# Kernel optimization log

Measured on AMD Instinct MI355X. Metric: run time of the kernel, lower is better.

## Reference

```python
import jax, jax.numpy as jnp
import numpy as np
import math

T, B, I, N, O = 512, 256, 128, 1024, 10
H_STEP = 0.1
ALPHA = 1.0
OMEGA = 1.0
GAMMA = 0.1
OMEGA_FACTOR = OMEGA * OMEGA
GAMMA_FACTOR = 2.0 * GAMMA
GAIN_REC = 1.0 / math.sqrt(N)


def setup_inputs() -> dict:
    key = jax.random.key(0)
    ks = jax.random.split(key, 7)
    # torch.nn.Linear default init: U(-1/sqrt(fan_in), 1/sqrt(fan_in))
    def lin(kw, kb, fan_out, fan_in):
        bound = 1.0 / math.sqrt(fan_in)
        w = jax.random.uniform(kw, (fan_out, fan_in), minval=-bound, maxval=bound, dtype=jnp.float32)
        b = jax.random.uniform(kb, (fan_out,), minval=-bound, maxval=bound, dtype=jnp.float32)
        return w, b
    i2h_w, i2h_b = lin(ks[0], ks[1], N, I)
    h2h_w, h2h_b = lin(ks[2], ks[3], N, N)
    h2o_w, h2o_b = lin(ks[4], ks[5], O, N)
    batch = jax.random.normal(ks[6], (T, B, I), dtype=jnp.float32)
    return {
        "batch": batch,
        "i2h_w": i2h_w, "i2h_b": i2h_b,
        "h2h_w": h2h_w, "h2h_b": h2h_b,
        "h2o_w": h2o_w, "h2o_b": h2o_b,
    }


def reference(batch, i2h_w, i2h_b, h2h_w, h2h_b, h2o_w, h2o_b):
    # Precompute input projection for all timesteps: [T, B, N]
    inp_proj = jnp.einsum('tbi,ni->tbn', batch, i2h_w) + i2h_b

    def step(carry, u_t):
        x_t, y_t = carry  # each [B, N]
        rec = GAIN_REC * (y_t @ h2h_w.T + h2h_b)  # gain scales full h2h(y) incl. bias
        y_t = y_t + H_STEP * (ALPHA * jnp.tanh(u_t + rec)
                              - OMEGA_FACTOR * x_t - GAMMA_FACTOR * y_t)
        x_t = x_t + H_STEP * y_t
        return (x_t, y_t), None

    x0 = jnp.zeros((batch.shape[1], h2h_w.shape[0]), dtype=batch.dtype)
    y0 = jnp.zeros_like(x0)
    (x_T, _), _ = jax.lax.scan(step, (x0, y0), inp_proj)
    output = x_T @ h2o_w.T + h2o_b  # [B, O]
    return output
```

## Files before the change

kernel.cpp:

```cpp
#include <hip/hip_runtime.h>

#define T_STEPS 512
#define BATCH_N 256
#define IDIM    128
#define NDIM    1024
#define ODIM    10

#define AGRP 16
#define BSLC 16
#define BB   16
#define NS   64
#define THREADS 256
#define GAIN 0.03125f

#define BATCH_BYTES (33554432ull)
#define YBUF_OFF    (33554432ull)
#define YBUF_HALF   (524288ull)
#define SEQ_OFF     (YBUF_OFF + 2*YBUF_HALF)
#define SEQ_BYTES   (4096ull)
#define XT_OFF      (SEQ_OFF + SEQ_BYTES)
#define XT_BYTES    (1048576ull)
#define WS_NEED     (XT_OFF + XT_BYTES)

typedef short    s16x8 __attribute__((ext_vector_type(8)));
typedef float    f32x4 __attribute__((ext_vector_type(4)));
typedef unsigned u32x4 __attribute__((ext_vector_type(4)));

__device__ __forceinline__ unsigned short f2bf(float f) {
  unsigned u = __builtin_bit_cast(unsigned, f);
  u += 0x7fffu + ((u >> 16) & 1u);
  return (unsigned short)(u >> 16);
}

__global__ void horn_convert(const float* __restrict__ src, unsigned short* __restrict__ dst) {
  size_t gid = (size_t)blockIdx.x * 256 + threadIdx.x;
  const f32x4* s4 = reinterpret_cast<const f32x4*>(src) + gid * 2;
  f32x4 a = s4[0], b = s4[1];
  u32x4 o;
  o[0] = (unsigned)f2bf(a[0]) | ((unsigned)f2bf(a[1]) << 16);
  o[1] = (unsigned)f2bf(a[2]) | ((unsigned)f2bf(a[3]) << 16);
  o[2] = (unsigned)f2bf(b[0]) | ((unsigned)f2bf(b[1]) << 16);
  o[3] = (unsigned)f2bf(b[2]) | ((unsigned)f2bf(b[3]) << 16);
  reinterpret_cast<u32x4*>(dst)[gid] = o;
}

__launch_bounds__(THREADS, 1)
__global__ void horn_persistent(const unsigned short* __restrict__ batchbf,
                                const float* __restrict__ i2h_w,
                                const float* __restrict__ i2h_b,
                                const float* __restrict__ h2h_w,
                                const float* __restrict__ h2h_b,
                                unsigned short* ybuf,
                                unsigned int*  seq,
                                float* xT)
{
  __shared__ char smem[32768];
  const int tid  = threadIdx.x;
  const int lane = tid & 63;
  const int wv   = tid >> 6;
  const int blk  = blockIdx.x;
  const int ig   = blk & 15;
  const int jg   = blk >> 4;
  const int l15  = lane & 15;
  const int kb   = lane >> 4;
  const int jc   = jg * NS + wv * 16 + l15;

  s16x8 wfrag[32];
  #pragma unroll
  for (int kc = 0; kc < 32; ++kc) {
    const f32x4* g = reinterpret_cast<const f32x4*>(h2h_w + (size_t)jc * NDIM + kc * 32 + kb * 8);
    f32x4 a = g[0], b = g[1];
    s16x8 v;
    v[0] = (short)f2bf(a[0]*GAIN); v[1] = (short)f2bf(a[1]*GAIN);
    v[2] = (short)f2bf(a[2]*GAIN); v[3] = (short)f2bf(a[3]*GAIN);
    v[4] = (short)f2bf(b[0]*GAIN); v[5] = (short)f2bf(b[1]*GAIN);
    v[6] = (short)f2bf(b[2]*GAIN); v[7] = (short)f2bf(b[3]*GAIN);
    wfrag[kc] = v;
  }

  s16x8 i2hf[4];
  #pragma unroll
  for (int kc = 0; kc < 4; ++kc) {
    const float* g = i2h_w + (size_t)jc * IDIM + kc * 32 + kb * 8;
    s16x8 v;
    #pragma unroll
    for (int e = 0; e < 8; ++e) v[e] = (short)f2bf(g[e]);
    i2hf[kc] = v;
  }
  const float bias = i2h_b[jc] + h2h_b[jc] * GAIN;

  s16x8 bfr[4];
  {
    const unsigned short* bp = batchbf + ((size_t)ig * BB + l15) * IDIM + kb * 8;
    #pragma unroll
    for (int kc = 0; kc < 4; ++kc) bfr[kc] = *reinterpret_cast<const s16x8*>(bp + kc * 32);
  }

  float xs[4] = {0.f,0.f,0.f,0.f};
  float ys[4] = {0.f,0.f,0.f,0.f};
  unsigned int* cnt = seq + ig * 32;

  for (int t = 0; t < T_STEPS; ++t) {
    if (t > 0) {
      const unsigned target = 64u * (unsigned)t;
      while (true) {
        unsigned v = 0;
        if (lane == 0) v = atomicAdd(cnt, 0u);
        v = (unsigned)__shfl((int)v, 0, 64);
        if (v >= target) break;
        __builtin_amdgcn_s_sleep(1);
      }
    }

    const char* gy = (const char*)ybuf + (size_t)(t & 1) * YBUF_HALF + (size_t)ig * (BB * NDIM * 2);
    const u32x4* g4 = reinterpret_cast<const u32x4*>(gy) + tid;
    u32x4 v0, v1, v2, v3, v4, v5, v6, v7;
    asm volatile(
      "global_load_dwordx4 %0, %8, off sc0 sc1\n\t"
      "global_load_dwordx4 %1, %9, off sc0 sc1\n\t"
      "global_load_dwordx4 %2, %10, off sc0 sc1\n\t"
      "global_load_dwordx4 %3, %11, off sc0 sc1\n\t"
      "global_load_dwordx4 %4, %12, off sc0 sc1\n\t"
      "global_load_dwordx4 %5, %13, off sc0 sc1\n\t"
      "global_load_dwordx4 %6, %14, off sc0 sc1\n\t"
      "global_load_dwordx4 %7, %15, off sc0 sc1"
      : "=&v"(v0), "=&v"(v1), "=&v"(v2), "=&v"(v3),
        "=&v"(v4), "=&v"(v5), "=&v"(v6), "=&v"(v7)
      : "v"(g4), "v"(g4+256), "v"(g4+512), "v"(g4+768),
        "v"(g4+1024), "v"(g4+1280), "v"(g4+1536), "v"(g4+1792)
      : "memory");

    f32x4 acc = {bias, bias, bias, bias};
    #pragma unroll
    for (int kc = 0; kc < 4; ++kc)
      acc = __builtin_amdgcn_mfma_f32_16x16x32_bf16(bfr[kc], i2hf[kc], acc, 0, 0, 0);

    asm volatile("s_waitcnt vmcnt(0)" ::: "memory");
    #define STG(r, vr) { int idx = tid + (r)*256; \
      *reinterpret_cast<u32x4*>(smem + ((idx*16) ^ (((idx>>7)&7)<<4))) = vr; }
    STG(0, v0) STG(1, v1) STG(2, v2) STG(3, v3)
    STG(4, v4) STG(5, v5) STG(6, v6) STG(7, v7)
    #undef STG
    __syncthreads();

    {
      const int tn = (t + 1 < T_STEPS) ? (t + 1) : t;
      const unsigned short* bp = batchbf + ((size_t)tn * BATCH_N + ig * BB + l15) * IDIM + kb * 8;
      #pragma unroll
      for (int kc = 0; kc < 4; ++kc) bfr[kc] = *reinterpret_cast<const s16x8*>(bp + kc * 32);
    }

    {
      const char* ybase = smem + l15 * 2048;
      const int swz = (l15 & 7) << 4;
      #pragma unroll
      for (int kc = 0; kc < 32; ++kc) {
        int ko = kc * 64 + kb * 16;
        s16x8 a = *reinterpret_cast<const s16x8*>(ybase + (ko ^ swz));
        acc = __builtin_amdgcn_mfma_f32_16x16x32_bf16(a, wfrag[kc], acc, 0, 0, 0);
      }
    }

    unsigned yw0, yw1, yw2, yw3;
    {
      float z, th, yn;
      z = acc[0]; th = tanhf(z); yn = ys[0] + 0.1f*(th - xs[0] - 0.2f*ys[0]); xs[0] += 0.1f*yn; ys[0] = yn; yw0 = f2bf(yn);
      z = acc[1]; th = tanhf(z); yn = ys[1] + 0.1f*(th - xs[1] - 0.2f*ys[1]); xs[1] += 0.1f*yn; ys[1] = yn; yw1 = f2bf(yn);
      z = acc[2]; th = tanhf(z); yn = ys[2] + 0.1f*(th - xs[2] - 0.2f*ys[2]); xs[2] += 0.1f*yn; ys[2] = yn; yw2 = f2bf(yn);
      z = acc[3]; th = tanhf(z); yn = ys[3] + 0.1f*(th - xs[3] - 0.2f*ys[3]); xs[3] += 0.1f*yn; ys[3] = yn; yw3 = f2bf(yn);
    }

    {
      unsigned short* wp = ybuf + (size_t)((t + 1) & 1) * 262144 + (size_t)ig * (BB * NDIM) + jc;
      asm volatile(
        "global_store_short %4, %0, off sc0 sc1\n\t"
        "global_store_short %5, %1, off sc0 sc1\n\t"
        "global_store_short %6, %2, off sc0 sc1\n\t"
        "global_store_short %7, %3, off sc0 sc1\n\t"
        "s_waitcnt vmcnt(0)"
        :
        : "v"(yw0), "v"(yw1), "v"(yw2), "v"(yw3),
          "v"(wp + (size_t)(kb*4+0)*NDIM), "v"(wp + (size_t)(kb*4+1)*NDIM),
          "v"(wp + (size_t)(kb*4+2)*NDIM), "v"(wp + (size_t)(kb*4+3)*NDIM)
        : "memory");
    }
    if (lane == 0) atomicAdd(cnt, 1u);
  }

  #pragma unroll
  for (int q = 0; q < 4; ++q) {
    int row = ig * BB + kb * 4 + q;
    xT[(size_t)row * NDIM + jc] = xs[q];
  }
}

__global__ void horn_out(const float* __restrict__ xT, const float* __restrict__ h2o_w,
                         const float* __restrict__ h2o_b, float* __restrict__ out) {
  int b = blockIdx.x;
  int lane = threadIdx.x;
  float p[ODIM];
  #pragma unroll
  for (int o = 0; o < ODIM; ++o) p[o] = 0.f;
  for (int it = 0; it < NDIM / 64; ++it) {
    int n = it * 64 + lane;
    float xv = xT[(size_t)b * NDIM + n];
    #pragma unroll
    for (int o = 0; o < ODIM; ++o) p[o] += xv * h2o_w[o * NDIM + n];
  }
  #pragma unroll
  for (int o = 0; o < ODIM; ++o) {
    float v = p[o];
    #pragma unroll
    for (int off = 32; off >= 1; off >>= 1) v += __shfl_down(v, off, 64);
    if (lane == 0) out[b * ODIM + o] = v + h2o_b[o];
  }
}

__global__ void horn_fail(float* out) {
  int i = blockIdx.x * 256 + threadIdx.x;
  if (i < BATCH_N * ODIM) out[i] = 12345.0f;
}

extern "C" void kernel_launch(void* const* d_in, const int* in_sizes, int n_in,
                              void* d_out, int out_size, void* d_ws, size_t ws_size,
                              hipStream_t stream) {
  const float* batch = (const float*)d_in[0];
  const float* i2h_w = (const float*)d_in[1];
  const float* i2h_b = (const float*)d_in[2];
  const float* h2h_w = (const float*)d_in[3];
  const float* h2h_b = (const float*)d_in[4];
  const float* h2o_w = (const float*)d_in[5];
  const float* h2o_b = (const float*)d_in[6];
  float* out = (float*)d_out;
  char* ws = (char*)d_ws;

  if (ws_size < WS_NEED) {
    horn_fail<<<16, 256, 0, stream>>>(out);
    return;
  }

  hipMemsetAsync(ws + YBUF_OFF, 0, YBUF_HALF, stream);
  hipMemsetAsync(ws + SEQ_OFF, 0, SEQ_BYTES, stream);

  horn_convert<<<8192, 256, 0, stream>>>(batch, (unsigned short*)(ws + 0));

  horn_persistent<<<AGRP * BSLC, THREADS, 0, stream>>>(
      (const unsigned short*)(ws + 0), i2h_w, i2h_b, h2h_w, h2h_b,
      (unsigned short*)(ws + YBUF_OFF), (unsigned int*)(ws + SEQ_OFF),
      (float*)(ws + XT_OFF));

  horn_out<<<BATCH_N, 64, 0, stream>>>((const float*)(ws + XT_OFF), h2o_w, h2o_b, out);
}
```

Baseline: 1.583 ms.

## Split recurrent K across waves with LDS reduction and per-wave flag barrier

Each wave now covers a quarter of the K dimension for all 64 output columns of the block. It loads its y slice straight from global memory into MFMA operands, skipping the LDS staging copy, and partial sums are reduced through a double-buffered LDS array. The shared atomic counter barrier is replaced by per-wave flag words that all 64 lanes poll together, so the atomic read-modify-write and the sleep are gone. tanhf is replaced by an exp/rcp formulation. Together these aim to shorten each recurrent step's critical path of sync, load and compute, at the cost of an extra LDS reduction and slightly lower tanh accuracy.

Result: slower. 4.251 ms (+168.6%).

```diff
diff --git a/kernel.cpp b/kernel.cpp
--- a/kernel.cpp
+++ b/kernel.cpp
@@ -6,19 +6,16 @@
 #define NDIM    1024
 #define ODIM    10
 
-#define AGRP 16
-#define BSLC 16
 #define BB   16
 #define NS   64
 #define THREADS 256
 #define GAIN 0.03125f
 
-#define BATCH_BYTES (33554432ull)
 #define YBUF_OFF    (33554432ull)
 #define YBUF_HALF   (524288ull)
-#define SEQ_OFF     (YBUF_OFF + 2*YBUF_HALF)
-#define SEQ_BYTES   (4096ull)
-#define XT_OFF      (SEQ_OFF + SEQ_BYTES)
+#define FLG_OFF     (YBUF_OFF + 2*YBUF_HALF)
+#define FLG_BYTES   (4096ull)
+#define XT_OFF      (FLG_OFF + FLG_BYTES)
 #define XT_BYTES    (1048576ull)
 #define WS_NEED     (XT_OFF + XT_BYTES)
 
@@ -51,10 +48,10 @@
                                 const float* __restrict__ h2h_w,
                                 const float* __restrict__ h2h_b,
                                 unsigned short* ybuf,
-                                unsigned int*  seq,
+                                unsigned int*  flags,
                                 float* xT)
 {
-  __shared__ char smem[32768];
+  __shared__ f32x4 red[2][16][64];
   const int tid  = threadIdx.x;
   const int lane = tid & 63;
   const int wv   = tid >> 6;
@@ -65,17 +62,21 @@
   const int kb   = lane >> 4;
   const int jc   = jg * NS + wv * 16 + l15;
 
-  s16x8 wfrag[32];
-  #pragma unroll
-  for (int kc = 0; kc < 32; ++kc) {
-    const f32x4* g = reinterpret_cast<const f32x4*>(h2h_w + (size_t)jc * NDIM + kc * 32 + kb * 8);
-    f32x4 a = g[0], b = g[1];
-    s16x8 v;
-    v[0] = (short)f2bf(a[0]*GAIN); v[1] = (short)f2bf(a[1]*GAIN);
-    v[2] = (short)f2bf(a[2]*GAIN); v[3] = (short)f2bf(a[3]*GAIN);
-    v[4] = (short)f2bf(b[0]*GAIN); v[5] = (short)f2bf(b[1]*GAIN);
-    v[6] = (short)f2bf(b[2]*GAIN); v[7] = (short)f2bf(b[3]*GAIN);
-    wfrag[kc] = v;
+  s16x8 wfrag[4][8];
+  #pragma unroll
+  for (int ct = 0; ct < 4; ++ct) {
+    #pragma unroll
+    for (int q = 0; q < 8; ++q) {
+      const float* g = h2h_w + (size_t)(jg * NS + ct * 16 + l15) * NDIM + wv * 256 + q * 32 + kb * 8;
+      f32x4 a = *reinterpret_cast<const f32x4*>(g);
+      f32x4 b = *reinterpret_cast<const f32x4*>(g + 4);
+      s16x8 v;
+      v[0] = (short)f2bf(a[0]*GAIN); v[1] = (short)f2bf(a[1]*GAIN);
+      v[2] = (short)f2bf(a[2]*GAIN); v[3] = (short)f2bf(a[3]*GAIN);
+      v[4] = (short)f2bf(b[0]*GAIN); v[5] = (short)f2bf(b[1]*GAIN);
+      v[6] = (short)f2bf(b[2]*GAIN); v[7] = (short)f2bf(b[3]*GAIN);
+      wfrag[ct][q] = v;
+    }
   }
 
   s16x8 i2hf[4];
@@ -96,52 +97,102 @@
     for (int kc = 0; kc < 4; ++kc) bfr[kc] = *reinterpret_cast<const s16x8*>(bp + kc * 32);
   }
 
+  const char* ybase = (const char*)ybuf + (size_t)ig * (BB * NDIM * 2)
+                      + (size_t)l15 * 2048 + wv * 512 + kb * 16;
+  unsigned short* wp0 = ybuf + (size_t)ig * (BB * NDIM) + (size_t)(kb * 4) * NDIM + jc;
+  const unsigned int* fpoll = flags + ig * 64 + lane;
+  unsigned int* fstore = flags + ig * 64 + jg * 4 + wv;
+
   float xs[4] = {0.f,0.f,0.f,0.f};
   float ys[4] = {0.f,0.f,0.f,0.f};
-  unsigned int* cnt = seq + ig * 32;
 
   for (int t = 0; t < T_STEPS; ++t) {
     if (t > 0) {
-      const unsigned target = 64u * (unsigned)t;
       while (true) {
-        unsigned v = 0;
-        if (lane == 0) v = atomicAdd(cnt, 0u);
-        v = (unsigned)__shfl((int)v, 0, 64);
-        if (v >= target) break;
-        __builtin_amdgcn_s_sleep(1);
+        unsigned fv;
+        asm volatile("global_load_dword %0, %1, off sc0 sc1\n\t"
+                     "s_waitcnt vmcnt(0)"
+                     : "=v"(fv) : "v"(fpoll) : "memory");
+        if (__all((int)fv >= t)) break;
       }
     }
 
-    const char* gy = (const char*)ybuf + (size_t)(t & 1) * YBUF_HALF + (size_t)ig * (BB * NDIM * 2);
-    const u32x4* g4 = reinterpret_cast<const u32x4*>(gy) + tid;
-    u32x4 v0, v1, v2, v3, v4, v5, v6, v7;
+    const char* gp = ybase + (size_t)(t & 1) * YBUF_HALF;
+    s16x8 a0, a1, a2, a3, a4, a5, a6, a7;
     asm volatile(
-      "global_load_dwordx4 %0, %8, off sc0 sc1\n\t"
-      "global_load_dwordx4 %1, %9, off sc0 sc1\n\t"
-      "global_load_dwordx4 %2, %10, off sc0 sc1\n\t"
-      "global_load_dwordx4 %3, %11, off sc0 sc1\n\t"
-      "global_load_dwordx4 %4, %12, off sc0 sc1\n\t"
-      "global_load_dwordx4 %5, %13, off sc0 sc1\n\t"
-      "global_load_dwordx4 %6, %14, off sc0 sc1\n\t"
-      "global_load_dwordx4 %7, %15, off sc0 sc1"
-      : "=&v"(v0), "=&v"(v1), "=&v"(v2), "=&v"(v3),
-        "=&v"(v4), "=&v"(v5), "=&v"(v6), "=&v"(v7)
-      : "v"(g4), "v"(g4+256), "v"(g4+512), "v"(g4+768),
-        "v"(g4+1024), "v"(g4+1280), "v"(g4+1536), "v"(g4+1792)
-      : "memory");
-
-    f32x4 acc = {bias, bias, bias, bias};
+      "global_load_dwordx4 %0, %8, off offset:0   sc0 sc1\n\t"
+      "global_load_dwordx4 %1, %8, off offset:64  sc0 sc1\n\t"
+      "global_load_dwordx4 %2, %8, off offset:128 sc0 sc1\n\t"
+      "global_load_dwordx4 %3, %8, off offset:192 sc0 sc1\n\t"
+      "global_load_dwordx4 %4, %8, off offset:256 sc0 sc1\n\t"
+      "global_load_dwordx4 %5, %8, off offset:320 sc0 sc1\n\t"
+      "global_load_dwordx4 %6, %8, off offset:384 sc0 sc1\n\t"
+      "global_load_dwordx4 %7, %8, off offset:448 sc0 sc1"
+      : "=&v"(a0), "=&v"(a1), "=&v"(a2), "=&v"(a3),
+        "=&v"(a4), "=&v"(a5), "=&v"(a6), "=&v"(a7)
+      : "v"(gp) : "memory");
+
+    f32x4 uacc = {bias, bias, bias, bias};
     #pragma unroll
     for (int kc = 0; kc < 4; ++kc)
-      acc = __builtin_amdgcn_mfma_f32_16x16x32_bf16(bfr[kc], i2hf[kc], acc, 0, 0, 0);
+      uacc = __builtin_amdgcn_mfma_f32_16x16x32_bf16(bfr[kc], i2hf[kc], uacc, 0, 0, 0);
 
     asm volatile("s_waitcnt vmcnt(0)" ::: "memory");
-    #define STG(r, vr) { int idx = tid + (r)*256; \
-      *reinterpret_cast<u32x4*>(smem + ((idx*16) ^ (((idx>>7)&7)<<4))) = vr; }
-    STG(0, v0) STG(1, v1) STG(2, v2) STG(3, v3)
-    STG(4, v4) STG(5, v5) STG(6, v6) STG(7, v7)
-    #undef STG
+    __builtin_amdgcn_sched_barrier(0);
+
+    f32x4 c0 = {0,0,0,0}, c1 = {0,0,0,0}, c2 = {0,0,0,0}, c3 = {0,0,0,0};
+    #define RECQ(aq, q) \
+      c0 = __builtin_amdgcn_mfma_f32_16x16x32_bf16(aq, wfrag[0][q], c0, 0, 0, 0); \
+      c1 = __builtin_amdgcn_mfma_f32_16x16x32_bf16(aq, wfrag[1][q], c1, 0, 0, 0); \
+      c2 = __builtin_amdgcn_mfma_f32_16x16x32_bf16(aq, wfrag[2][q], c2, 0, 0, 0); \
+      c3 = __builtin_amdgcn_mfma_f32_16x16x32_bf16(aq, wfrag[3][q], c3, 0, 0, 0);
+    RECQ(a0, 0) RECQ(a1, 1) RECQ(a2, 2) RECQ(a3, 3)
+    RECQ(a4, 4) RECQ(a5, 5) RECQ(a6, 6) RECQ(a7, 7)
+    #undef RECQ
+
+    const int rp = t & 1;
+    red[rp][wv * 4 + 0][lane] = c0;
+    red[rp][wv * 4 + 1][lane] = c1;
+    red[rp][wv * 4 + 2][lane] = c2;
+    red[rp][wv * 4 + 3][lane] = c3;
     __syncthreads();
+    f32x4 z4 = uacc;
+    z4 += red[rp][0 * 4 + wv][lane];
+    z4 += red[rp][1 * 4 + wv][lane];
+    z4 += red[rp][2 * 4 + wv][lane];
+    z4 += red[rp][3 * 4 + wv][lane];
+
+    unsigned yw0, yw1, yw2, yw3;
+    {
+      float z, e, r, th, yn;
+      z = z4[0]; e = __expf(z + z); r = __builtin_amdgcn_rcpf(e + 1.0f); th = fmaf(-2.0f, r, 1.0f);
+      yn = ys[0] + 0.1f*(th - xs[0] - 0.2f*ys[0]); xs[0] += 0.1f*yn; ys[0] = yn; yw0 = f2bf(yn);
+      z = z4[1]; e = __expf(z + z); r = __builtin_amdgcn_rcpf(e + 1.0f); th = fmaf(-2.0f, r, 1.0f);
+      yn = ys[1] + 0.1f*(th - xs[1] - 0.2f*ys[1]); xs[1] += 0.1f*yn; ys[1] = yn; yw1 = f2bf(yn);
+      z = z4[2]; e = __expf(z + z); r = __builtin_amdgcn_rcpf(e + 1.0f); th = fmaf(-2.0f, r, 1.0f);
+      yn = ys[2] + 0.1f*(th - xs[2] - 0.2f*ys[2]); xs[2] += 0.1f*yn; ys[2] = yn; yw2 = f2bf(yn);
+      z = z4[3]; e = __expf(z + z); r = __builtin_amdgcn_rcpf(e + 1.0f); th = fmaf(-2.0f, r, 1.0f);
+      yn = ys[3] + 0.1f*(th - xs[3] - 0.2f*ys[3]); xs[3] += 0.1f*yn; ys[3] = yn; yw3 = f2bf(yn);
+    }
+
+    {
+      unsigned short* b0 = wp0 + (size_t)((t + 1) & 1) * 262144;
+      unsigned short* b1 = b0 + 2 * NDIM;
+      asm volatile(
+        "global_store_short %4, %0, off offset:0    sc0 sc1\n\t"
+        "global_store_short %4, %1, off offset:2048 sc0 sc1\n\t"
+        "global_store_short %5, %2, off offset:0    sc0 sc1\n\t"
+        "global_store_short %5, %3, off offset:2048 sc0 sc1\n\t"
+        "s_waitcnt vmcnt(0)"
+        :
+        : "v"(yw0), "v"(yw1), "v"(yw2), "v"(yw3), "v"(b0), "v"(b1)
+        : "memory");
+    }
+    if (lane == 0) {
+      unsigned nv = (unsigned)(t + 1);
+      asm volatile("global_store_dword %0, %1, off sc0 sc1"
+                   :: "v"(fstore), "v"(nv) : "memory");
+    }
 
     {
       const int tn = (t + 1 < T_STEPS) ? (t + 1) : t;
@@ -149,42 +200,6 @@
       #pragma unroll
       for (int kc = 0; kc < 4; ++kc) bfr[kc] = *reinterpret_cast<const s16x8*>(bp + kc * 32);
     }
-
-    {
-      const char* ybase = smem + l15 * 2048;
-      const int swz = (l15 & 7) << 4;
-      #pragma unroll
-      for (int kc = 0; kc < 32; ++kc) {
-        int ko = kc * 64 + kb * 16;
-        s16x8 a = *reinterpret_cast<const s16x8*>(ybase + (ko ^ swz));
-        acc = __builtin_amdgcn_mfma_f32_16x16x32_bf16(a, wfrag[kc], acc, 0, 0, 0);
-      }
-    }
-
-    unsigned yw0, yw1, yw2, yw3;
-    {
-      float z, th, yn;
-      z = acc[0]; th = tanhf(z); yn = ys[0] + 0.1f*(th - xs[0] - 0.2f*ys[0]); xs[0] += 0.1f*yn; ys[0] = yn; yw0 = f2bf(yn);
-      z = acc[1]; th = tanhf(z); yn = ys[1] + 0.1f*(th - xs[1] - 0.2f*ys[1]); xs[1] += 0.1f*yn; ys[1] = yn; yw1 = f2bf(yn);
-      z = acc[2]; th = tanhf(z); yn = ys[2] + 0.1f*(th - xs[2] - 0.2f*ys[2]); xs[2] += 0.1f*yn; ys[2] = yn; yw2 = f2bf(yn);
-      z = acc[3]; th = tanhf(z); yn = ys[3] + 0.1f*(th - xs[3] - 0.2f*ys[3]); xs[3] += 0.1f*yn; ys[3] = yn; yw3 = f2bf(yn);
-    }
-
-    {
-      unsigned short* wp = ybuf + (size_t)((t + 1) & 1) * 262144 + (size_t)ig * (BB * NDIM) + jc;
-      asm volatile(
-        "global_store_short %4, %0, off sc0 sc1\n\t"
-        "global_store_short %5, %1, off sc0 sc1\n\t"
-        "global_store_short %6, %2, off sc0 sc1\n\t"
-        "global_store_short %7, %3, off sc0 sc1\n\t"
-        "s_waitcnt vmcnt(0)"
-        :
-        : "v"(yw0), "v"(yw1), "v"(yw2), "v"(yw3),
-          "v"(wp + (size_t)(kb*4+0)*NDIM), "v"(wp + (size_t)(kb*4+1)*NDIM),
-          "v"(wp + (size_t)(kb*4+2)*NDIM), "v"(wp + (size_t)(kb*4+3)*NDIM)
-        : "memory");
-    }
-    if (lane == 0) atomicAdd(cnt, 1u);
   }
 
   #pragma unroll
@@ -240,13 +255,13 @@
   }
 
   hipMemsetAsync(ws + YBUF_OFF, 0, YBUF_HALF, stream);
-  hipMemsetAsync(ws + SEQ_OFF, 0, SEQ_BYTES, stream);
+  hipMemsetAsync(ws + FLG_OFF, 0, FLG_BYTES, stream);
 
   horn_convert<<<8192, 256, 0, stream>>>(batch, (unsigned short*)(ws + 0));
 
-  horn_persistent<<<AGRP * BSLC, THREADS, 0, stream>>>(
+  horn_persistent<<<256, THREADS, 0, stream>>>(
       (const unsigned short*)(ws + 0), i2h_w, i2h_b, h2h_w, h2h_b,
-      (unsigned short*)(ws + YBUF_OFF), (unsigned int*)(ws + SEQ_OFF),
+      (unsigned short*)(ws + YBUF_OFF), (unsigned int*)(ws + FLG_OFF),
       (float*)(ws + XT_OFF));
 
   horn_out<<<BATCH_N, 64, 0, stream>>>((const float*)(ws + XT_OFF), h2o_w, h2o_b, out);
```

## Replace atomic counter barrier with per-element tagged flags and split-K across waves

Applied to the files above, without the earlier changes.

Each y value is now stored as a 32-bit word holding the bf16 value and a timestep tag. Consumers poll their own y slice until every tag reaches the current step, which removes the separate atomic counter and the store-then-signal ordering. The work split changes to 128 blocks of 128 columns, with each wave taking a quarter of K. Partial sums are reduced through double-buffered LDS instead of staging y in LDS. tanh becomes an exp/rcp approximation; the cost is double the y traffic and a higher risk from per-element polling.

Measured after the change: 2.589 ms. +63.6%, slower.

```diff
diff --git a/kernel.cpp b/kernel.cpp
--- a/kernel.cpp
+++ b/kernel.cpp
@@ -6,19 +6,12 @@
 #define NDIM    1024
 #define ODIM    10
 
-#define AGRP 16
-#define BSLC 16
-#define BB   16
-#define NS   64
 #define THREADS 256
 #define GAIN 0.03125f
 
-#define BATCH_BYTES (33554432ull)
 #define YBUF_OFF    (33554432ull)
-#define YBUF_HALF   (524288ull)
-#define SEQ_OFF     (YBUF_OFF + 2*YBUF_HALF)
-#define SEQ_BYTES   (4096ull)
-#define XT_OFF      (SEQ_OFF + SEQ_BYTES)
+#define YBUF_WORDS  (2ull*16*16*1024)
+#define XT_OFF      (YBUF_OFF + YBUF_WORDS*4ull)
 #define XT_BYTES    (1048576ull)
 #define WS_NEED     (XT_OFF + XT_BYTES)
 
@@ -31,6 +24,7 @@
   u += 0x7fffu + ((u >> 16) & 1u);
   return (unsigned short)(u >> 16);
 }
+__device__ __forceinline__ unsigned umin2(unsigned a, unsigned b) { return a < b ? a : b; }
 
 __global__ void horn_convert(const float* __restrict__ src, unsigned short* __restrict__ dst) {
   size_t gid = (size_t)blockIdx.x * 256 + threadIdx.x;
@@ -50,147 +44,166 @@
                                 const float* __restrict__ i2h_b,
                                 const float* __restrict__ h2h_w,
                                 const float* __restrict__ h2h_b,
-                                unsigned short* ybuf,
-                                unsigned int*  seq,
+                                unsigned* ybuf,
                                 float* xT)
 {
-  __shared__ char smem[32768];
+  __shared__ f32x4 red[2][4][8][64];
   const int tid  = threadIdx.x;
   const int lane = tid & 63;
   const int wv   = tid >> 6;
-  const int blk  = blockIdx.x;
-  const int ig   = blk & 15;
-  const int jg   = blk >> 4;
+  const int ig   = blockIdx.x & 15;
+  const int jg   = blockIdx.x >> 4;
   const int l15  = lane & 15;
   const int kb   = lane >> 4;
-  const int jc   = jg * NS + wv * 16 + l15;
-
-  s16x8 wfrag[32];
-  #pragma unroll
-  for (int kc = 0; kc < 32; ++kc) {
-    const f32x4* g = reinterpret_cast<const f32x4*>(h2h_w + (size_t)jc * NDIM + kc * 32 + kb * 8);
-    f32x4 a = g[0], b = g[1];
+
+  s16x8 wfrag[8][8];
+  #pragma unroll
+  for (int ct = 0; ct < 8; ++ct) {
+    #pragma unroll
+    for (int kc = 0; kc < 8; ++kc) {
+      const float* g = h2h_w + (size_t)(jg * 128 + ct * 16 + l15) * NDIM + wv * 256 + kc * 32 + kb * 8;
+      f32x4 a = *reinterpret_cast<const f32x4*>(g);
+      f32x4 b = *reinterpret_cast<const f32x4*>(g + 4);
+      s16x8 v;
+      v[0] = (short)f2bf(a[0]*GAIN); v[1] = (short)f2bf(a[1]*GAIN);
+      v[2] = (short)f2bf(a[2]*GAIN); v[3] = (short)f2bf(a[3]*GAIN);
+      v[4] = (short)f2bf(b[0]*GAIN); v[5] = (short)f2bf(b[1]*GAIN);
+      v[6] = (short)f2bf(b[2]*GAIN); v[7] = (short)f2bf(b[3]*GAIN);
+      wfrag[ct][kc] = v;
+    }
+  }
+
+  s16x8 i2hf[8];
+  #pragma unroll
+  for (int ct = 0; ct < 8; ++ct) {
+    const float* g = i2h_w + (size_t)(jg * 128 + ct * 16 + l15) * IDIM + wv * 32 + kb * 8;
     s16x8 v;
-    v[0] = (short)f2bf(a[0]*GAIN); v[1] = (short)f2bf(a[1]*GAIN);
-    v[2] = (short)f2bf(a[2]*GAIN); v[3] = (short)f2bf(a[3]*GAIN);
-    v[4] = (short)f2bf(b[0]*GAIN); v[5] = (short)f2bf(b[1]*GAIN);
-    v[6] = (short)f2bf(b[2]*GAIN); v[7] = (short)f2bf(b[3]*GAIN);
-    wfrag[kc] = v;
-  }
-
-  s16x8 i2hf[4];
-  #pragma unroll
-  for (int kc = 0; kc < 4; ++kc) {
-    const float* g = i2h_w + (size_t)jc * IDIM + kc * 32 + kb * 8;
-    s16x8 v;
     #pragma unroll
     for (int e = 0; e < 8; ++e) v[e] = (short)f2bf(g[e]);
-    i2hf[kc] = v;
-  }
-  const float bias = i2h_b[jc] + h2h_b[jc] * GAIN;
-
-  s16x8 bfr[4];
-  {
-    const unsigned short* bp = batchbf + ((size_t)ig * BB + l15) * IDIM + kb * 8;
-    #pragma unroll
-    for (int kc = 0; kc < 4; ++kc) bfr[kc] = *reinterpret_cast<const s16x8*>(bp + kc * 32);
-  }
-
-  float xs[4] = {0.f,0.f,0.f,0.f};
-  float ys[4] = {0.f,0.f,0.f,0.f};
-  unsigned int* cnt = seq + ig * 32;
+    i2hf[ct] = v;
+  }
+
+  const int c0 = jg * 128 + (2 * wv) * 16 + l15;
+  const int c1 = c0 + 16;
+  const float bias0 = i2h_b[c0] + GAIN * h2h_b[c0];
+  const float bias1 = i2h_b[c1] + GAIN * h2h_b[c1];
+
+  s16x8 bfr = *reinterpret_cast<const s16x8*>(
+      batchbf + ((size_t)ig * 16 + l15) * IDIM + wv * 32 + kb * 8);
+
+  float xs[8] = {0,0,0,0,0,0,0,0};
+  float ys[8] = {0,0,0,0,0,0,0,0};
+
+  const unsigned* gbase = ybuf + ((size_t)ig * 16 + l15) * 1024 + wv * 256 + kb * 8;
 
   for (int t = 0; t < T_STEPS; ++t) {
-    if (t > 0) {
-      const unsigned target = 64u * (unsigned)t;
-      while (true) {
-        unsigned v = 0;
-        if (lane == 0) v = atomicAdd(cnt, 0u);
-        v = (unsigned)__shfl((int)v, 0, 64);
-        if (v >= target) break;
-        __builtin_amdgcn_s_sleep(1);
-      }
+    f32x4 c0a = __builtin_amdgcn_mfma_f32_16x16x32_bf16(bfr, i2hf[0], (f32x4){0,0,0,0}, 0, 0, 0);
+    f32x4 c1a = __builtin_amdgcn_mfma_f32_16x16x32_bf16(bfr, i2hf[1], (f32x4){0,0,0,0}, 0, 0, 0);
+    f32x4 c2a = __builtin_amdgcn_mfma_f32_16x16x32_bf16(bfr, i2hf[2], (f32x4){0,0,0,0}, 0, 0, 0);
+    f32x4 c3a = __builtin_amdgcn_mfma_f32_16x16x32_bf16(bfr, i2hf[3], (f32x4){0,0,0,0}, 0, 0, 0);
+    f32x4 c4a = __builtin_amdgcn_mfma_f32_16x16x32_bf16(bfr, i2hf[4], (f32x4){0,0,0,0}, 0, 0, 0);
+    f32x4 c5a = __builtin_amdgcn_mfma_f32_16x16x32_bf16(bfr, i2hf[5], (f32x4){0,0,0,0}, 0, 0, 0);
+    f32x4 c6a = __builtin_amdgcn_mfma_f32_16x16x32_bf16(bfr, i2hf[6], (f32x4){0,0,0,0}, 0, 0, 0);
+    f32x4 c7a = __builtin_amdgcn_mfma_f32_16x16x32_bf16(bfr, i2hf[7], (f32x4){0,0,0,0}, 0, 0, 0);
+
+    const unsigned* gp = gbase + (size_t)(t & 1) * 262144;
+    u32x4 g0,g1,g2,g3,g4,g5,g6,g7,g8,g9,g10,g11,g12,g13,g14,g15;
+    while (true) {
+      asm volatile(
+        "global_load_dwordx4 %0, %16, off offset:0 sc0 sc1\n\t"
+        "global_load_dwordx4 %1, %16, off offset:16 sc0 sc1\n\t"
+        "global_load_dwordx4 %2, %16, off offset:128 sc0 sc1\n\t"
+        "global_load_dwordx4 %3, %16, off offset:144 sc0 sc1\n\t"
+        "global_load_dwordx4 %4, %16, off offset:256 sc0 sc1\n\t"
+        "global_load_dwordx4 %5, %16, off offset:272 sc0 sc1\n\t"
+        "global_load_dwordx4 %6, %16, off offset:384 sc0 sc1\n\t"
+        "global_load_dwordx4 %7, %16, off offset:400 sc0 sc1\n\t"
+        "global_load_dwordx4 %8, %16, off offset:512 sc0 sc1\n\t"
+        "global_load_dwordx4 %9, %16, off offset:528 sc0 sc1\n\t"
+        "global_load_dwordx4 %10, %16, off offset:640 sc0 sc1\n\t"
+        "global_load_dwordx4 %11, %16, off offset:656 sc0 sc1\n\t"
+        "global_load_dwordx4 %12, %16, off offset:768 sc0 sc1\n\t"
+        "global_load_dwordx4 %13, %16, off offset:784 sc0 sc1\n\t"
+        "global_load_dwordx4 %14, %16, off offset:896 sc0 sc1\n\t"
+        "global_load_dwordx4 %15, %16, off offset:912 sc0 sc1\n\t"
+        "s_waitcnt vmcnt(0)"
+        : "=&v"(g0), "=&v"(g1), "=&v"(g2), "=&v"(g3),
+          "=&v"(g4), "=&v"(g5), "=&v"(g6), "=&v"(g7),
+          "=&v"(g8), "=&v"(g9), "=&v"(g10), "=&v"(g11),
+          "=&v"(g12), "=&v"(g13), "=&v"(g14), "=&v"(g15)
+        : "v"(gp) : "memory");
+      unsigned mn = 0xffffffffu;
+      #define MN(v) mn = umin2(mn, umin2(umin2(v[0]&0xffffu, v[1]&0xffffu), umin2(v[2]&0xffffu, v[3]&0xffffu)));
+      MN(g0) MN(g1) MN(g2) MN(g3) MN(g4) MN(g5) MN(g6) MN(g7)
+      MN(g8) MN(g9) MN(g10) MN(g11) MN(g12) MN(g13) MN(g14) MN(g15)
+      #undef MN
+      if (__all((int)(mn >= (unsigned)t))) break;
+      __builtin_amdgcn_s_sleep(2);
     }
 
-    const char* gy = (const char*)ybuf + (size_t)(t & 1) * YBUF_HALF + (size_t)ig * (BB * NDIM * 2);
-    const u32x4* g4 = reinterpret_cast<const u32x4*>(gy) + tid;
-    u32x4 v0, v1, v2, v3, v4, v5, v6, v7;
-    asm volatile(
-      "global_load_dwordx4 %0, %8, off sc0 sc1\n\t"
-      "global_load_dwordx4 %1, %9, off sc0 sc1\n\t"
-      "global_load_dwordx4 %2, %10, off sc0 sc1\n\t"
-      "global_load_dwordx4 %3, %11, off sc0 sc1\n\t"
-      "global_load_dwordx4 %4, %12, off sc0 sc1\n\t"
-      "global_load_dwordx4 %5, %13, off sc0 sc1\n\t"
-      "global_load_dwordx4 %6, %14, off sc0 sc1\n\t"
-      "global_load_dwordx4 %7, %15, off sc0 sc1"
-      : "=&v"(v0), "=&v"(v1), "=&v"(v2), "=&v"(v3),
-        "=&v"(v4), "=&v"(v5), "=&v"(v6), "=&v"(v7)
-      : "v"(g4), "v"(g4+256), "v"(g4+512), "v"(g4+768),
-        "v"(g4+1024), "v"(g4+1280), "v"(g4+1536), "v"(g4+1792)
-      : "memory");
-
-    f32x4 acc = {bias, bias, bias, bias};
-    #pragma unroll
-    for (int kc = 0; kc < 4; ++kc)
-      acc = __builtin_amdgcn_mfma_f32_16x16x32_bf16(bfr[kc], i2hf[kc], acc, 0, 0, 0);
-
-    asm volatile("s_waitcnt vmcnt(0)" ::: "memory");
-    #define STG(r, vr) { int idx = tid + (r)*256; \
-      *reinterpret_cast<u32x4*>(smem + ((idx*16) ^ (((idx>>7)&7)<<4))) = vr; }
-    STG(0, v0) STG(1, v1) STG(2, v2) STG(3, v3)
-    STG(4, v4) STG(5, v5) STG(6, v6) STG(7, v7)
-    #undef STG
+    s16x8 a0, a1, a2, a3, a4, a5, a6, a7;
+    #define RPK(dst, lo, hi) { u32x4 o_; \
+      o_[0] = __builtin_amdgcn_perm(lo[1], lo[0], 0x07060302u); \
+      o_[1] = __builtin_amdgcn_perm(lo[3], lo[2], 0x07060302u); \
+      o_[2] = __builtin_amdgcn_perm(hi[1], hi[0], 0x07060302u); \
+      o_[3] = __builtin_amdgcn_perm(hi[3], hi[2], 0x07060302u); \
+      dst = __builtin_bit_cast(s16x8, o_); }
+    RPK(a0, g0, g1)   RPK(a1, g2, g3)   RPK(a2, g4, g5)   RPK(a3, g6, g7)
+    RPK(a4, g8, g9)   RPK(a5, g10, g11) RPK(a6, g12, g13) RPK(a7, g14, g15)
+    #undef RPK
+
+    #define RECK(ak, kc) \
+      c0a = __builtin_amdgcn_mfma_f32_16x16x32_bf16(ak, wfrag[0][kc], c0a, 0, 0, 0); \
+      c1a = __builtin_amdgcn_mfma_f32_16x16x32_bf16(ak, wfrag[1][kc], c1a, 0, 0, 0); \
+      c2a = __builtin_amdgcn_mfma_f32_16x16x32_bf16(ak, wfrag[2][kc], c2a, 0, 0, 0); \
+      c3a = __builtin_amdgcn_mfma_f32_16x16x32_bf16(ak, wfrag[3][kc], c3a, 0, 0, 0); \
+      c4a = __builtin_amdgcn_mfma_f32_16x16x32_bf16(ak, wfrag[4][kc], c4a, 0, 0, 0); \
+      c5a = __builtin_amdgcn_mfma_f32_16x16x32_bf16(ak, wfrag[5][kc], c5a, 0, 0, 0); \
+      c6a = __builtin_amdgcn_mfma_f32_16x16x32_bf16(ak, wfrag[6][kc], c6a, 0, 0, 0); \
+      c7a = __builtin_amdgcn_mfma_f32_16x16x32_bf16(ak, wfrag[7][kc], c7a, 0, 0, 0);
+    RECK(a0, 0) RECK(a1, 1) RECK(a2, 2) RECK(a3, 3)
+    RECK(a4, 4) RECK(a5, 5) RECK(a6, 6) RECK(a7, 7)
+    #undef RECK
+
+    const int rp = t & 1;
+    red[rp][wv][0][lane] = c0a; red[rp][wv][1][lane] = c1a;
+    red[rp][wv][2][lane] = c2a; red[rp][wv][3][lane] = c3a;
+    red[rp][wv][4][lane] = c4a; red[rp][wv][5][lane] = c5a;
+    red[rp][wv][6][lane] = c6a; red[rp][wv][7][lane] = c7a;
     __syncthreads();
+    f32x4 z0 = red[rp][0][2*wv][lane]   + red[rp][1][2*wv][lane]
+             + red[rp][2][2*wv][lane]   + red[rp][3][2*wv][lane];
+    f32x4 z1 = red[rp][0][2*wv+1][lane] + red[rp][1][2*wv+1][lane]
+             + red[rp][2][2*wv+1][lane] + red[rp][3][2*wv+1][lane];
+
+    const unsigned tag = (unsigned)(t + 1);
+    unsigned* pb = ybuf + (size_t)((t + 1) & 1) * 262144 + (size_t)ig * 16384 + (size_t)(kb * 4) * 1024;
+    #define UPD(s, r, zv, biasv, colv) { \
+      float z_ = zv[r] + biasv; \
+      float e_ = __expf(z_ + z_); \
+      float th_ = fmaf(-2.0f, __builtin_amdgcn_rcpf(e_ + 1.0f), 1.0f); \
+      int si_ = (s)*4 + (r); \
+      float yn_ = ys[si_] + 0.1f*(th_ - xs[si_] - 0.2f*ys[si_]); \
+      xs[si_] += 0.1f*yn_; ys[si_] = yn_; \
+      unsigned w_ = ((unsigned)f2bf(yn_) << 16) | tag; \
+      unsigned* ad_ = pb + (r) * 1024 + (colv); \
+      asm volatile("global_store_dword %0, %1, off sc0 sc1" :: "v"(ad_), "v"(w_) : "memory"); }
+    UPD(0, 0, z0, bias0, c0) UPD(0, 1, z0, bias0, c0) UPD(0, 2, z0, bias0, c0) UPD(0, 3, z0, bias0, c0)
+    UPD(1, 0, z1, bias1, c1) UPD(1, 1, z1, bias1, c1) UPD(1, 2, z1, bias1, c1) UPD(1, 3, z1, bias1, c1)
+    #undef UPD
 
     {
       const int tn = (t + 1 < T_STEPS) ? (t + 1) : t;
-      const unsigned short* bp = batchbf + ((size_t)tn * BATCH_N + ig * BB + l15) * IDIM + kb * 8;
-      #pragma unroll
-      for (int kc = 0; kc < 4; ++kc) bfr[kc] = *reinterpret_cast<const s16x8*>(bp + kc * 32);
+      bfr = *reinterpret_cast<const s16x8*>(
+          batchbf + ((size_t)tn * BATCH_N + ig * 16 + l15) * IDIM + wv * 32 + kb * 8);
     }
-
-    {
-      const char* ybase = smem + l15 * 2048;
-      const int swz = (l15 & 7) << 4;
-      #pragma unroll
-      for (int kc = 0; kc < 32; ++kc) {
-        int ko = kc * 64 + kb * 16;
-        s16x8 a = *reinterpret_cast<const s16x8*>(ybase + (ko ^ swz));
-        acc = __builtin_amdgcn_mfma_f32_16x16x32_bf16(a, wfrag[kc], acc, 0, 0, 0);
-      }
-    }
-
-    unsigned yw0, yw1, yw2, yw3;
-    {
-      float z, th, yn;
-      z = acc[0]; th = tanhf(z); yn = ys[0] + 0.1f*(th - xs[0] - 0.2f*ys[0]); xs[0] += 0.1f*yn; ys[0] = yn; yw0 = f2bf(yn);
-      z = acc[1]; th = tanhf(z); yn = ys[1] + 0.1f*(th - xs[1] - 0.2f*ys[1]); xs[1] += 0.1f*yn; ys[1] = yn; yw1 = f2bf(yn);
-      z = acc[2]; th = tanhf(z); yn = ys[2] + 0.1f*(th - xs[2] - 0.2f*ys[2]); xs[2] += 0.1f*yn; ys[2] = yn; yw2 = f2bf(yn);
-      z = acc[3]; th = tanhf(z); yn = ys[3] + 0.1f*(th - xs[3] - 0.2f*ys[3]); xs[3] += 0.1f*yn; ys[3] = yn; yw3 = f2bf(yn);
-    }
-
-    {
-      unsigned short* wp = ybuf + (size_t)((t + 1) & 1) * 262144 + (size_t)ig * (BB * NDIM) + jc;
-      asm volatile(
-        "global_store_short %4, %0, off sc0 sc1\n\t"
-        "global_store_short %5, %1, off sc0 sc1\n\t"
-        "global_store_short %6, %2, off sc0 sc1\n\t"
-        "global_store_short %7, %3, off sc0 sc1\n\t"
-        "s_waitcnt vmcnt(0)"
-        :
-        : "v"(yw0), "v"(yw1), "v"(yw2), "v"(yw3),
-          "v"(wp + (size_t)(kb*4+0)*NDIM), "v"(wp + (size_t)(kb*4+1)*NDIM),
-          "v"(wp + (size_t)(kb*4+2)*NDIM), "v"(wp + (size_t)(kb*4+3)*NDIM)
-        : "memory");
-    }
-    if (lane == 0) atomicAdd(cnt, 1u);
-  }
-
-  #pragma unroll
-  for (int q = 0; q < 4; ++q) {
-    int row = ig * BB + kb * 4 + q;
-    xT[(size_t)row * NDIM + jc] = xs[q];
+  }
+
+  #pragma unroll
+  for (int r = 0; r < 4; ++r) {
+    int row = ig * 16 + kb * 4 + r;
+    xT[(size_t)row * NDIM + c0] = xs[r];
+    xT[(size_t)row * NDIM + c1] = xs[4 + r];
   }
 }
 
@@ -239,15 +252,13 @@
     return;
   }
 
-  hipMemsetAsync(ws + YBUF_OFF, 0, YBUF_HALF, stream);
-  hipMemsetAsync(ws + SEQ_OFF, 0, SEQ_BYTES, stream);
+  hipMemsetAsync(ws + YBUF_OFF, 0, YBUF_WORDS * 4, stream);
 
   horn_convert<<<8192, 256, 0, stream>>>(batch, (unsigned short*)(ws + 0));
 
-  horn_persistent<<<AGRP * BSLC, THREADS, 0, stream>>>(
+  horn_persistent<<<128, THREADS, 0, stream>>>(
       (const unsigned short*)(ws + 0), i2h_w, i2h_b, h2h_w, h2h_b,
-      (unsigned short*)(ws + YBUF_OFF), (unsigned int*)(ws + SEQ_OFF),
-      (float*)(ws + XT_OFF));
+      (unsigned*)(ws + YBUF_OFF), (float*)(ws + XT_OFF));
 
   horn_out<<<BATCH_N, 64, 0, stream>>>((const float*)(ws + XT_OFF), h2o_w, h2o_b, out);
 }
```
